# Kernel tuning notes

Hardware: AMD Instinct MI355X
Metric: run time of the kernel (lower is better)

## Reference

```python
import jax, jax.numpy as jnp
import numpy as np

EMB = 1024
HEADS = 16
HEAD_DIM = EMB // HEADS
FF = 4 * EMB


def _gelu_tanh(x):
    c = jnp.sqrt(jnp.asarray(2.0 / jnp.pi, x.dtype))
    return 0.5 * x * (1.0 + jnp.tanh(c * (x + 0.044715 * x ** 3)))


def _layernorm(x, scale, shift, eps=1e-5):
    mean = jnp.mean(x, axis=-1, keepdims=True)
    var = jnp.mean((x - mean) ** 2, axis=-1, keepdims=True)
    return scale * (x - mean) / jnp.sqrt(var + eps) + shift


def setup_inputs() -> dict:
    key = jax.random.key(0)
    ks = jax.random.split(key, 8)
    s = 0.02
    return {
        "x": jax.random.normal(ks[0], (2, 2048, EMB), jnp.float32),
        "w_q": jax.random.normal(ks[1], (EMB, EMB), jnp.float32) * s,
        "w_k": jax.random.normal(ks[2], (EMB, EMB), jnp.float32) * s,
        "w_v": jax.random.normal(ks[3], (EMB, EMB), jnp.float32) * s,
        "w_o": jax.random.normal(ks[4], (EMB, EMB), jnp.float32) * s,
        "b_o": jnp.zeros((EMB,), jnp.float32),
        "ln1_scale": jnp.ones((EMB,), jnp.float32),
        "ln1_shift": jnp.zeros((EMB,), jnp.float32),
        "ln2_scale": jnp.ones((EMB,), jnp.float32),
        "ln2_shift": jnp.zeros((EMB,), jnp.float32),
        "w_ff1": jax.random.normal(ks[5], (EMB, FF), jnp.float32) * s,
        "b_ff1": jnp.zeros((FF,), jnp.float32),
        "w_ff2": jax.random.normal(ks[6], (FF, EMB), jnp.float32) * s,
        "b_ff2": jnp.zeros((EMB,), jnp.float32),
    }


def _attention(x, w_q, w_k, w_v, w_o, b_o):
    b, n, _ = x.shape
    q = (x @ w_q).reshape(b, n, HEADS, HEAD_DIM).transpose(0, 2, 1, 3)  # bhnd
    k = (x @ w_k).reshape(b, n, HEADS, HEAD_DIM).transpose(0, 2, 1, 3)
    v = (x @ w_v).reshape(b, n, HEADS, HEAD_DIM).transpose(0, 2, 1, 3)
    scores = jnp.einsum("bhqd,bhkd->bhqk", q, k)
    causal = jnp.triu(jnp.ones((n, n), bool), k=1)
    scores = jnp.where(causal, -jnp.inf, scores)
    # original scales AFTER masking (-inf stays -inf)
    attn = jax.nn.softmax(scores / jnp.sqrt(jnp.asarray(HEAD_DIM, x.dtype)), axis=-1)
    ctx = jnp.einsum("bhqk,bhkd->bhqd", attn, v)
    ctx = ctx.transpose(0, 2, 1, 3).reshape(b, n, EMB)
    return ctx @ w_o + b_o


def reference(x, w_q, w_k, w_v, w_o, b_o, ln1_scale, ln1_shift,
              ln2_scale, ln2_shift, w_ff1, b_ff1, w_ff2, b_ff2):
    h = _layernorm(x, ln1_scale, ln1_shift)
    h = _attention(h, w_q, w_k, w_v, w_o, b_o)
    x = x + h  # dropout is identity at drop_rate=0 / eval
    h = _layernorm(x, ln2_scale, ln2_shift)
    h = _gelu_tanh(h @ w_ff1 + b_ff1) @ w_ff2 + b_ff2
    return x + h
```

## Files before the change

### kernel.cpp

```cpp
#include <hip/hip_runtime.h>
#include <math.h>

#define EMB 1024
#define HEADS 16
#define HD 64
#define FF_DIM 4096
#define SEQ 2048
#define BATCH 2
#define NTOK (BATCH * SEQ)

typedef __bf16 bf16x8 __attribute__((ext_vector_type(8)));
typedef float f32x4 __attribute__((ext_vector_type(4)));

__device__ __forceinline__ unsigned short f2bf(float f) {
    union { float f; unsigned int u; } v; v.f = f;
    unsigned int r = v.u + 0x7fff + ((v.u >> 16) & 1);
    return (unsigned short)(r >> 16);
}

__device__ __forceinline__ float gelu_f(float x) {
    const float c = 0.7978845608028654f;
    float x3 = x * x * x;
    return 0.5f * x * (1.f + tanhf(c * (x + 0.044715f * x3)));
}

#define GLOAD_LDS16(g, l)                                                      \
    __builtin_amdgcn_global_load_lds(                                          \
        (const __attribute__((address_space(1))) void*)(g),                    \
        (__attribute__((address_space(3))) void*)(l), 16, 0, 0)

__global__ __launch_bounds__(256) void ln_kernel(const float* __restrict__ x,
                                                 const float* __restrict__ scale,
                                                 const float* __restrict__ shift,
                                                 unsigned short* __restrict__ out) {
    int row = blockIdx.x;
    const float* xr = x + (size_t)row * EMB;
    unsigned short* yr = out + (size_t)row * EMB;
    int t = threadIdx.x;

    float v[4];
    float s = 0.f, s2 = 0.f;
#pragma unroll
    for (int i = 0; i < 4; i++) {
        v[i] = xr[t + i * 256];
        s += v[i];
        s2 += v[i] * v[i];
    }
    for (int o = 32; o > 0; o >>= 1) {
        s += __shfl_down(s, o, 64);
        s2 += __shfl_down(s2, o, 64);
    }
    __shared__ float red[4], red2[4];
    int wave = t >> 6;
    if ((t & 63) == 0) { red[wave] = s; red2[wave] = s2; }
    __syncthreads();
    if (t == 0) {
        float a = 0.f, b = 0.f;
#pragma unroll
        for (int i = 0; i < 4; i++) { a += red[i]; b += red2[i]; }
        red[0] = a; red2[0] = b;
    }
    __syncthreads();
    float mean = red[0] * (1.f / EMB);
    float var = red2[0] * (1.f / EMB) - mean * mean;
    float rstd = rsqrtf(var + 1e-5f);
#pragma unroll
    for (int i = 0; i < 4; i++) {
        int c = t + i * 256;
        yr[c] = f2bf(scale[c] * (v[i] - mean) * rstd + shift[c]);
    }
}

__global__ __launch_bounds__(256) void transpose_cast6(
    const float* __restrict__ w0, const float* __restrict__ w1,
    const float* __restrict__ w2, const float* __restrict__ w3,
    const float* __restrict__ w4, const float* __restrict__ w5,
    unsigned short* __restrict__ o0, unsigned short* __restrict__ o1,
    unsigned short* __restrict__ o2, unsigned short* __restrict__ o3,
    unsigned short* __restrict__ o4, unsigned short* __restrict__ o5) {
    __shared__ float tile[64][65];
    int id = blockIdx.x;
    const float* src; unsigned short* dst; int K, N, lid;
    if (id < 256)       { src = w0; dst = o0; K = 1024; N = 1024; lid = id; }
    else if (id < 512)  { src = w1; dst = o1; K = 1024; N = 1024; lid = id - 256; }
    else if (id < 768)  { src = w2; dst = o2; K = 1024; N = 1024; lid = id - 512; }
    else if (id < 1024) { src = w3; dst = o3; K = 1024; N = 1024; lid = id - 768; }
    else if (id < 2048) { src = w4; dst = o4; K = 1024; N = 4096; lid = id - 1024; }
    else                { src = w5; dst = o5; K = 4096; N = 1024; lid = id - 2048; }
    int tn = N >> 6;
    int k0 = (lid / tn) << 6, n0 = (lid % tn) << 6;
    int t = threadIdx.x;
    int rr = t >> 6, cc = t & 63;
#pragma unroll
    for (int i = 0; i < 16; i++) {
        int r = i * 4 + rr;
        tile[r][cc] = src[(size_t)(k0 + r) * N + n0 + cc];
    }
    __syncthreads();
#pragma unroll
    for (int i = 0; i < 16; i++) {
        int r = i * 4 + rr;
        dst[(size_t)(n0 + r) * K + k0 + cc] = f2bf(tile[cc][r]);
    }
}

template <int EPI>
__global__ __launch_bounds__(256) void mfma_gemm(
    const unsigned short* __restrict__ A,
    const unsigned short* __restrict__ Bt,
    void* __restrict__ Cv,
    const float* __restrict__ bias,
    const float* __restrict__ resid,
    int M, int N, int K) {
    __shared__ unsigned short As[128 * 32];
    __shared__ unsigned short Bs[128 * 32];

    const int t = threadIdx.x;
    const int w = t >> 6, lane = t & 63;
    const int m0 = blockIdx.y * 128, n0 = blockIdx.x * 128;

    const int sr0 = (w << 5) + (lane >> 2);
    const int sr1 = sr0 + 16;
    const int p = lane & 3;
    const int c0 = p ^ ((sr0 >> 1) & 3);
    const int c1 = p ^ ((sr1 >> 1) & 3);
    const unsigned short* gA0 = A + (size_t)(m0 + sr0) * K + c0 * 8;
    const unsigned short* gA1 = A + (size_t)(m0 + sr1) * K + c1 * 8;
    const unsigned short* gB0 = Bt + (size_t)(n0 + sr0) * K + c0 * 8;
    const unsigned short* gB1 = Bt + (size_t)(n0 + sr1) * K + c1 * 8;
    unsigned short* lA0 = &As[(w << 5) * 32];
    unsigned short* lA1 = &As[((w << 5) + 16) * 32];
    unsigned short* lB0 = &Bs[(w << 5) * 32];
    unsigned short* lB1 = &Bs[((w << 5) + 16) * 32];

    const int mrow = (w >> 1) * 64, ncol = (w & 1) * 64;
    int aoff[4], boff[4];
#pragma unroll
    for (int i = 0; i < 4; i++) {
        int ra = mrow + i * 16 + (lane & 15);
        int pa = (lane >> 4) ^ ((ra >> 1) & 3);
        aoff[i] = ra * 32 + pa * 8;
        int rb = ncol + i * 16 + (lane & 15);
        int pb = (lane >> 4) ^ ((rb >> 1) & 3);
        boff[i] = rb * 32 + pb * 8;
    }

    f32x4 acc[4][4];
#pragma unroll
    for (int i = 0; i < 4; i++)
#pragma unroll
        for (int j = 0; j < 4; j++) acc[i][j] = (f32x4){0.f, 0.f, 0.f, 0.f};

    for (int k0 = 0; k0 < K; k0 += 32) {
        __syncthreads();
        GLOAD_LDS16(gA0, lA0);
        GLOAD_LDS16(gA1, lA1);
        GLOAD_LDS16(gB0, lB0);
        GLOAD_LDS16(gB1, lB1);
        gA0 += 32; gA1 += 32; gB0 += 32; gB1 += 32;
        __syncthreads();

        bf16x8 af[4], bfr[4];
#pragma unroll
        for (int i = 0; i < 4; i++) {
            af[i] = *reinterpret_cast<const bf16x8*>(&As[aoff[i]]);
            bfr[i] = *reinterpret_cast<const bf16x8*>(&Bs[boff[i]]);
        }
#pragma unroll
        for (int i = 0; i < 4; i++)
#pragma unroll
            for (int j = 0; j < 4; j++)
                acc[i][j] = __builtin_amdgcn_mfma_f32_16x16x32_bf16(
                    af[i], bfr[j], acc[i][j], 0, 0, 0);
    }

    const int ccol = lane & 15;
    const int crow = (lane >> 4) << 2;
#pragma unroll
    for (int i = 0; i < 4; i++) {
#pragma unroll
        for (int j = 0; j < 4; j++) {
            int col = n0 + ncol + j * 16 + ccol;
#pragma unroll
            for (int r = 0; r < 4; r++) {
                int row = m0 + mrow + i * 16 + crow + r;
                size_t idx = (size_t)row * N + col;
                float val = acc[i][j][r];
                if constexpr (EPI == 1) {
                    ((float*)Cv)[idx] = val + bias[col] + resid[idx];
                } else {
                    ((unsigned short*)Cv)[idx] = f2bf(gelu_f(val + bias[col]));
                }
            }
        }
    }
}

__global__ __launch_bounds__(256) void mfma_gemm_pk(
    const unsigned short* __restrict__ A,
    const unsigned short* __restrict__ Bt,
    float* __restrict__ P,
    int M, int N, int K) {
    __shared__ unsigned short As[128 * 32];
    __shared__ unsigned short Bs[128 * 32];

    const int t = threadIdx.x;
    const int w = t >> 6, lane = t & 63;
    const int m0 = blockIdx.y * 128, n0 = blockIdx.x * 128;
    const int kc = K / gridDim.z;
    const int kbeg = blockIdx.z * kc;

    const int sr0 = (w << 5) + (lane >> 2);
    const int sr1 = sr0 + 16;
    const int pp = lane & 3;
    const int c0 = pp ^ ((sr0 >> 1) & 3);
    const int c1 = pp ^ ((sr1 >> 1) & 3);
    const unsigned short* gA0 = A + (size_t)(m0 + sr0) * K + kbeg + c0 * 8;
    const unsigned short* gA1 = A + (size_t)(m0 + sr1) * K + kbeg + c1 * 8;
    const unsigned short* gB0 = Bt + (size_t)(n0 + sr0) * K + kbeg + c0 * 8;
    const unsigned short* gB1 = Bt + (size_t)(n0 + sr1) * K + kbeg + c1 * 8;
    unsigned short* lA0 = &As[(w << 5) * 32];
    unsigned short* lA1 = &As[((w << 5) + 16) * 32];
    unsigned short* lB0 = &Bs[(w << 5) * 32];
    unsigned short* lB1 = &Bs[((w << 5) + 16) * 32];

    const int mrow = (w >> 1) * 64, ncol = (w & 1) * 64;
    int aoff[4], boff[4];
#pragma unroll
    for (int i = 0; i < 4; i++) {
        int ra = mrow + i * 16 + (lane & 15);
        int pa = (lane >> 4) ^ ((ra >> 1) & 3);
        aoff[i] = ra * 32 + pa * 8;
        int rb = ncol + i * 16 + (lane & 15);
        int pb = (lane >> 4) ^ ((rb >> 1) & 3);
        boff[i] = rb * 32 + pb * 8;
    }

    f32x4 acc[4][4];
#pragma unroll
    for (int i = 0; i < 4; i++)
#pragma unroll
        for (int j = 0; j < 4; j++) acc[i][j] = (f32x4){0.f, 0.f, 0.f, 0.f};

    for (int k0 = 0; k0 < kc; k0 += 32) {
        __syncthreads();
        GLOAD_LDS16(gA0, lA0);
        GLOAD_LDS16(gA1, lA1);
        GLOAD_LDS16(gB0, lB0);
        GLOAD_LDS16(gB1, lB1);
        gA0 += 32; gA1 += 32; gB0 += 32; gB1 += 32;
        __syncthreads();

        bf16x8 af[4], bfr[4];
#pragma unroll
        for (int i = 0; i < 4; i++) {
            af[i] = *reinterpret_cast<const bf16x8*>(&As[aoff[i]]);
            bfr[i] = *reinterpret_cast<const bf16x8*>(&Bs[boff[i]]);
        }
#pragma unroll
        for (int i = 0; i < 4; i++)
#pragma unroll
            for (int j = 0; j < 4; j++)
                acc[i][j] = __builtin_amdgcn_mfma_f32_16x16x32_bf16(
                    af[i], bfr[j], acc[i][j], 0, 0, 0);
    }

    float* C = P + (size_t)blockIdx.z * M * N;
    const int ccol = lane & 15;
    const int crow = (lane >> 4) << 2;
#pragma unroll
    for (int i = 0; i < 4; i++) {
#pragma unroll
        for (int j = 0; j < 4; j++) {
            int col = n0 + ncol + j * 16 + ccol;
#pragma unroll
            for (int r = 0; r < 4; r++) {
                int row = m0 + mrow + i * 16 + crow + r;
                C[(size_t)row * N + col] = acc[i][j][r];
            }
        }
    }
}

__global__ __launch_bounds__(256) void oproj_reduce(
    float* __restrict__ out, const float* __restrict__ x,
    const float* __restrict__ p0, const float* __restrict__ p1,
    const float* __restrict__ bias) {
    int i = blockIdx.x * 256 + threadIdx.x;
    float4 xv = ((const float4*)x)[i];
    float4 a = ((const float4*)p0)[i];
    float4 b = ((const float4*)p1)[i];
    int c = (i * 4) & (EMB - 1);
    xv.x += a.x + b.x + bias[c];
    xv.y += a.y + b.y + bias[c + 1];
    xv.z += a.z + b.z + bias[c + 2];
    xv.w += a.w + b.w + bias[c + 3];
    ((float4*)out)[i] = xv;
}

__global__ __launch_bounds__(256) void ff2_reduce(
    float* __restrict__ out, const float* __restrict__ p0,
    const float* __restrict__ p1, const float* __restrict__ bias) {
    int i = blockIdx.x * 256 + threadIdx.x;
    float4 o = ((const float4*)out)[i];
    float4 a = ((const float4*)p0)[i];
    float4 b = ((const float4*)p1)[i];
    int c = (i * 4) & (EMB - 1);
    o.x += a.x + b.x + bias[c];
    o.y += a.y + b.y + bias[c + 1];
    o.z += a.z + b.z + bias[c + 2];
    o.w += a.w + b.w + bias[c + 3];
    ((float4*)out)[i] = o;
}

__global__ __launch_bounds__(256) void qkv_gemm(
    const unsigned short* __restrict__ lnO,
    const unsigned short* __restrict__ wqkT,
    const unsigned short* __restrict__ wvT,
    unsigned short* __restrict__ q,
    unsigned short* __restrict__ kb,
    unsigned short* __restrict__ vT) {
    __shared__ unsigned short As[128 * 32];
    __shared__ unsigned short Bs[128 * 32];

    const int t = threadIdx.x;
    const int w = t >> 6, lane = t & 63;
    const int bid = blockIdx.x;
    const bool qk = bid < 512;

    const unsigned short *A, *Bt;
    int m0, n0, N;
    if (qk) {
        A = lnO; Bt = wqkT;
        m0 = (bid >> 4) * 128; n0 = (bid & 15) * 128; N = 2048;
    } else {
        int lb = bid - 512;
        A = wvT; Bt = lnO;
        m0 = (lb & 7) * 128; n0 = (lb >> 3) * 128; N = 4096;
    }
    const int K = 1024;

    const int sr0 = (w << 5) + (lane >> 2);
    const int sr1 = sr0 + 16;
    const int p = lane & 3;
    const int c0 = p ^ ((sr0 >> 1) & 3);
    const int c1 = p ^ ((sr1 >> 1) & 3);
    const unsigned short* gA0 = A + (size_t)(m0 + sr0) * K + c0 * 8;
    const unsigned short* gA1 = A + (size_t)(m0 + sr1) * K + c1 * 8;
    const unsigned short* gB0 = Bt + (size_t)(n0 + sr0) * K + c0 * 8;
    const unsigned short* gB1 = Bt + (size_t)(n0 + sr1) * K + c1 * 8;
    unsigned short* lA0 = &As[(w << 5) * 32];
    unsigned short* lA1 = &As[((w << 5) + 16) * 32];
    unsigned short* lB0 = &Bs[(w << 5) * 32];
    unsigned short* lB1 = &Bs[((w << 5) + 16) * 32];

    const int mrow = (w >> 1) * 64, ncol = (w & 1) * 64;
    int aoff[4], boff[4];
#pragma unroll
    for (int i = 0; i < 4; i++) {
        int ra = mrow + i * 16 + (lane & 15);
        int pa = (lane >> 4) ^ ((ra >> 1) & 3);
        aoff[i] = ra * 32 + pa * 8;
        int rb = ncol + i * 16 + (lane & 15);
        int pb = (lane >> 4) ^ ((rb >> 1) & 3);
        boff[i] = rb * 32 + pb * 8;
    }

    f32x4 acc[4][4];
#pragma unroll
    for (int i = 0; i < 4; i++)
#pragma unroll
        for (int j = 0; j < 4; j++) acc[i][j] = (f32x4){0.f, 0.f, 0.f, 0.f};

    for (int k0 = 0; k0 < K; k0 += 32) {
        __syncthreads();
        GLOAD_LDS16(gA0, lA0);
        GLOAD_LDS16(gA1, lA1);
        GLOAD_LDS16(gB0, lB0);
        GLOAD_LDS16(gB1, lB1);
        gA0 += 32; gA1 += 32; gB0 += 32; gB1 += 32;
        __syncthreads();

        bf16x8 af[4], bfr[4];
#pragma unroll
        for (int i = 0; i < 4; i++) {
            af[i] = *reinterpret_cast<const bf16x8*>(&As[aoff[i]]);
            bfr[i] = *reinterpret_cast<const bf16x8*>(&Bs[boff[i]]);
        }
#pragma unroll
        for (int i = 0; i < 4; i++)
#pragma unroll
            for (int j = 0; j < 4; j++)
                acc[i][j] = __builtin_amdgcn_mfma_f32_16x16x32_bf16(
                    af[i], bfr[j], acc[i][j], 0, 0, 0);
    }

    const int ccol = lane & 15;
    const int crow = (lane >> 4) << 2;
    unsigned short* dst;
    int nbase;
    if (qk) {
        dst = (n0 < 1024) ? q : kb;
        nbase = n0 & 1023;
    } else {
        dst = vT;
        nbase = n0;
    }
    const int ldc = qk ? 1024 : 4096;
#pragma unroll
    for (int i = 0; i < 4; i++) {
#pragma unroll
        for (int j = 0; j < 4; j++) {
            int col = nbase + ncol + j * 16 + ccol;
#pragma unroll
            for (int r = 0; r < 4; r++) {
                int row = m0 + mrow + i * 16 + crow + r;
                dst[(size_t)row * ldc + col] = f2bf(acc[i][j][r]);
            }
        }
    }
}

__global__ __launch_bounds__(256) void attn_mfma(
    const unsigned short* __restrict__ Q,
    const unsigned short* __restrict__ K,
    const unsigned short* __restrict__ Vt,
    unsigned short* __restrict__ O) {
    __shared__ unsigned short Ks[2][64 * 64];
    __shared__ unsigned short Vs[2][64 * 64];
    __shared__ unsigned short Ps[4][16 * 64];

    const int t = threadIdx.x;
    const int w = t >> 6, lane = t & 63;
    const int l15 = lane & 15, l4 = lane >> 4;
    const int bh = blockIdx.y;
    const int b = bh >> 4, h = bh & 15;
    const int pair = blockIdx.x;

    const int sr = (w << 3) + (lane >> 3);
    const int sc = lane & 7;
    const int c = sc ^ (sr & 7);
    const unsigned short* kbase = K + ((size_t)(b * SEQ)) * EMB + h * HD;
    const unsigned short* vbase = Vt + ((size_t)(h * HD)) * (size_t)NTOK + (size_t)b * SEQ;
    unsigned short* Pw = &Ps[w][0];

#define STAGE(k0s, buf)                                                        \
    do {                                                                       \
        GLOAD_LDS16(kbase + (size_t)((k0s) + sr) * EMB + c * 8,                \
                    &Ks[buf][(w << 3) * 64]);                                  \
        GLOAD_LDS16(kbase + (size_t)((k0s) + sr + 32) * EMB + c * 8,           \
                    &Ks[buf][((w << 3) + 32) * 64]);                           \
        GLOAD_LDS16(vbase + (size_t)sr * NTOK + (k0s) + c * 8,                 \
                    &Vs[buf][(w << 3) * 64]);                                  \
        GLOAD_LDS16(vbase + (size_t)(sr + 32) * NTOK + (k0s) + c * 8,          \
                    &Vs[buf][((w << 3) + 32) * 64]);                           \
    } while (0)

    const float C1 = 0.125f * 1.4426950408889634f;
    const float C2 = 3.0f * 1.4426950408889634f;

#pragma unroll
    for (int phase = 0; phase < 2; phase++) {
        const int qt = phase ? pair : (31 - pair);
        const int q0 = qt * 64;

        const unsigned short* qg =
            Q + ((size_t)(b * SEQ + q0 + w * 16 + l15)) * EMB + h * HD + l4 * 8;
        bf16x8 qf0 = *(const bf16x8*)qg;
        bf16x8 qf1 = *(const bf16x8*)(qg + 32);
        const int qrow_c = q0 + w * 16 + l4 * 4;

        float lsum[4] = {0.f, 0.f, 0.f, 0.f};
        f32x4 Oacc[4];
#pragma unroll
        for (int j = 0; j < 4; j++) Oacc[j] = (f32x4){0.f, 0.f, 0.f, 0.f};

        const int ntiles = qt + 1;
        __syncthreads();
        STAGE(0, 0);
        for (int tile = 0; tile < ntiles; tile++) {
            const int k0 = tile * 64;
            const int buf = tile & 1;
            __syncthreads();
            if (tile + 1 < ntiles) STAGE(k0 + 64, buf ^ 1);

            f32x4 S[4];
#pragma unroll
            for (int j = 0; j < 4; j++) S[j] = (f32x4){0.f, 0.f, 0.f, 0.f};
#pragma unroll
            for (int s = 0; s < 2; s++) {
                bf16x8 qf = s ? qf1 : qf0;
#pragma unroll
                for (int j = 0; j < 4; j++) {
                    int rk = 16 * j + l15;
                    int phys = (s * 4 + l4) ^ (rk & 7);
                    bf16x8 kf = *(const bf16x8*)&Ks[buf][rk * 64 + phys * 8];
                    S[j] = __builtin_amdgcn_mfma_f32_16x16x32_bf16(qf, kf, S[j], 0, 0, 0);
                }
            }

            if (tile == ntiles - 1) {
#pragma unroll
                for (int j = 0; j < 4; j++)
#pragma unroll
                    for (int r = 0; r < 4; r++) {
                        float e = exp2f(S[j][r] * C1 - C2);
                        if (k0 + 16 * j + l15 > qrow_c + r) e = 0.f;
                        S[j][r] = e;
                        lsum[r] += e;
                    }
            } else {
#pragma unroll
                for (int j = 0; j < 4; j++)
#pragma unroll
                    for (int r = 0; r < 4; r++) {
                        float e = exp2f(S[j][r] * C1 - C2);
                        S[j][r] = e;
                        lsum[r] += e;
                    }
            }

#pragma unroll
            for (int r = 0; r < 4; r++) {
                int row = l4 * 4 + r;
#pragma unroll
                for (int j = 0; j < 4; j++) {
                    int col = 16 * j + l15;
                    int phys = (col >> 3) ^ (row & 7);
                    Pw[row * 64 + phys * 8 + (col & 7)] = f2bf(S[j][r]);
                }
            }

#pragma unroll
            for (int s = 0; s < 2; s++) {
                int pphys = (s * 4 + l4) ^ (l15 & 7);
                bf16x8 pf = *(const bf16x8*)&Pw[l15 * 64 + pphys * 8];
#pragma unroll
                for (int j = 0; j < 4; j++) {
                    int rv = 16 * j + l15;
                    int vphys = (s * 4 + l4) ^ (rv & 7);
                    bf16x8 vf = *(const bf16x8*)&Vs[buf][rv * 64 + vphys * 8];
                    Oacc[j] = __builtin_amdgcn_mfma_f32_16x16x32_bf16(pf, vf, Oacc[j], 0, 0, 0);
                }
            }
        }

#pragma unroll
        for (int r = 0; r < 4; r++) {
            float l = lsum[r];
#pragma unroll
            for (int off = 1; off < 16; off <<= 1)
                l += __shfl_xor(l, off, 64);
            float inv = 1.f / l;
            size_t rowb = (size_t)(b * SEQ + qrow_c + r) * EMB + h * HD;
#pragma unroll
            for (int j = 0; j < 4; j++)
                O[rowb + 16 * j + l15] = f2bf(Oacc[j][r] * inv);
        }
    }
#undef STAGE
}

extern "C" void kernel_launch(void* const* d_in, const int* in_sizes, int n_in,
                              void* d_out, int out_size, void* d_ws, size_t ws_size,
                              hipStream_t stream) {
    const float* x     = (const float*)d_in[0];
    const float* w_q   = (const float*)d_in[1];
    const float* w_k   = (const float*)d_in[2];
    const float* w_v   = (const float*)d_in[3];
    const float* w_o   = (const float*)d_in[4];
    const float* b_o   = (const float*)d_in[5];
    const float* ln1s  = (const float*)d_in[6];
    const float* ln1b  = (const float*)d_in[7];
    const float* ln2s  = (const float*)d_in[8];
    const float* ln2b  = (const float*)d_in[9];
    const float* w_ff1 = (const float*)d_in[10];
    const float* b_ff1 = (const float*)d_in[11];
    const float* w_ff2 = (const float*)d_in[12];
    const float* b_ff2 = (const float*)d_in[13];
    float* out = (float*)d_out;

    char* p = (char*)d_ws;
    unsigned short* lnO  = (unsigned short*)p; p += (size_t)NTOK * EMB * 2;
    unsigned short* q    = (unsigned short*)p; p += (size_t)NTOK * EMB * 2;
    unsigned short* kbuf = (unsigned short*)p; p += (size_t)NTOK * EMB * 2;
    unsigned short* vT   = (unsigned short*)p; p += (size_t)NTOK * EMB * 2;
    unsigned short* ctx  = (unsigned short*)p; p += (size_t)NTOK * EMB * 2;
    unsigned short* ff1a = (unsigned short*)p; p += (size_t)NTOK * FF_DIM * 2;
    unsigned short* wqkT = (unsigned short*)p; p += (size_t)2 * EMB * EMB * 2;
    unsigned short* wvT  = (unsigned short*)p; p += (size_t)EMB * EMB * 2;
    unsigned short* woT  = (unsigned short*)p; p += (size_t)EMB * EMB * 2;
    unsigned short* wf1T = (unsigned short*)p; p += (size_t)FF_DIM * EMB * 2;
    unsigned short* wf2T = (unsigned short*)p; p += (size_t)EMB * FF_DIM * 2;

    float* pbuf = (float*)lnO;

    dim3 blk(256);
    dim3 gOproj(EMB / 128, NTOK / 128, 2);
    dim3 gFF1(FF_DIM / 128, NTOK / 128);
    dim3 gFF2(EMB / 128, NTOK / 128, 2);
    dim3 gAttn(16, BATCH * HEADS);

    transpose_cast6<<<3072, blk, 0, stream>>>(
        w_q, w_k, w_v, w_o, w_ff1, w_ff2,
        wqkT, wqkT + (size_t)EMB * EMB, wvT, woT, wf1T, wf2T);
    ln_kernel<<<NTOK, blk, 0, stream>>>(x, ln1s, ln1b, lnO);
    qkv_gemm<<<768, blk, 0, stream>>>(lnO, wqkT, wvT, q, kbuf, vT);
    attn_mfma<<<gAttn, blk, 0, stream>>>(q, kbuf, vT, ctx);
    mfma_gemm_pk<<<gOproj, blk, 0, stream>>>(ctx, woT, pbuf, NTOK, EMB, EMB);
    oproj_reduce<<<NTOK * EMB / 4 / 256, blk, 0, stream>>>(
        out, x, pbuf, pbuf + (size_t)NTOK * EMB, b_o);
    ln_kernel<<<NTOK, blk, 0, stream>>>(out, ln2s, ln2b, lnO);
    mfma_gemm<2><<<gFF1, blk, 0, stream>>>(lnO, wf1T, ff1a, b_ff1, nullptr, NTOK, FF_DIM, EMB);
    mfma_gemm_pk<<<gFF2, blk, 0, stream>>>(ff1a, wf2T, pbuf, NTOK, EMB, FF_DIM);
    ff2_reduce<<<NTOK * EMB / 4 / 256, blk, 0, stream>>>(
        out, pbuf, pbuf + (size_t)NTOK * EMB, b_ff2);
}
```

Before: 397.9 us.

## Fuse o-proj reduction with LN2, use sigmoid GELU, split-K 4 for FF2

Replaces the o-proj partial reduction and the second layernorm with one kernel that sums partials, bias and residual, writes the residual, and emits the bf16 LN output. GELU is rewritten via the sigmoid identity with a fast exp and reciprocal. FF2 split-K is raised to 4 when the workspace has room for extra partial buffers, with a four-way reduce. This trades extra partial-sum traffic for more parallelism and saves a full activation round trip plus a launch.

```diff
diff --git a/kernel.cpp b/kernel.cpp
--- a/kernel.cpp
+++ b/kernel.cpp
@@ -19,9 +19,10 @@
 }
 
 __device__ __forceinline__ float gelu_f(float x) {
-    const float c = 0.7978845608028654f;
-    float x3 = x * x * x;
-    return 0.5f * x * (1.f + tanhf(c * (x + 0.044715f * x3)));
+    const float A = 1.5957691216057308f;
+    const float B = 0.07135481282989427f;
+    float zz = x * (A + B * x * x);
+    return x * __builtin_amdgcn_rcpf(1.f + __expf(-zz));
 }
 
 #define GLOAD_LDS16(g, l)                                                      \
@@ -68,6 +69,51 @@
     for (int i = 0; i < 4; i++) {
         int c = t + i * 256;
         yr[c] = f2bf(scale[c] * (v[i] - mean) * rstd + shift[c]);
+    }
+}
+
+__global__ __launch_bounds__(256) void oproj_ln(
+    const float* __restrict__ x, const float* __restrict__ p0,
+    const float* __restrict__ p1, const float* __restrict__ bo,
+    const float* __restrict__ scale, const float* __restrict__ shift,
+    float* __restrict__ out, unsigned short* __restrict__ ln2O) {
+    int row = blockIdx.x;
+    size_t rb = (size_t)row * EMB;
+    int t = threadIdx.x;
+
+    float v[4];
+    float s = 0.f, s2 = 0.f;
+#pragma unroll
+    for (int i = 0; i < 4; i++) {
+        int c = t + i * 256;
+        float val = x[rb + c] + p0[rb + c] + p1[rb + c] + bo[c];
+        out[rb + c] = val;
+        v[i] = val;
+        s += val;
+        s2 += val * val;
+    }
+    for (int o = 32; o > 0; o >>= 1) {
+        s += __shfl_down(s, o, 64);
+        s2 += __shfl_down(s2, o, 64);
+    }
+    __shared__ float red[4], red2[4];
+    int wave = t >> 6;
+    if ((t & 63) == 0) { red[wave] = s; red2[wave] = s2; }
+    __syncthreads();
+    if (t == 0) {
+        float a = 0.f, b = 0.f;
+#pragma unroll
+        for (int i = 0; i < 4; i++) { a += red[i]; b += red2[i]; }
+        red[0] = a; red2[0] = b;
+    }
+    __syncthreads();
+    float mean = red[0] * (1.f / EMB);
+    float var = red2[0] * (1.f / EMB) - mean * mean;
+    float rstd = rsqrtf(var + 1e-5f);
+#pragma unroll
+    for (int i = 0; i < 4; i++) {
+        int c = t + i * 256;
+        ln2O[rb + c] = f2bf(scale[c] * (v[i] - mean) * rstd + shift[c]);
     }
 }
 
@@ -199,7 +245,7 @@
 __global__ __launch_bounds__(256) void mfma_gemm_pk(
     const unsigned short* __restrict__ A,
     const unsigned short* __restrict__ Bt,
-    float* __restrict__ P,
+    float* __restrict__ P0, float* __restrict__ P1,
     int M, int N, int K) {
     __shared__ unsigned short As[128 * 32];
     __shared__ unsigned short Bs[128 * 32];
@@ -265,7 +311,8 @@
                     af[i], bfr[j], acc[i][j], 0, 0, 0);
     }
 
-    float* C = P + (size_t)blockIdx.z * M * N;
+    float* C = (blockIdx.z < 2) ? (P0 + (size_t)blockIdx.z * M * N)
+                                : (P1 + (size_t)(blockIdx.z - 2) * M * N);
     const int ccol = lane & 15;
     const int crow = (lane >> 4) << 2;
 #pragma unroll
@@ -282,23 +329,7 @@
     }
 }
 
-__global__ __launch_bounds__(256) void oproj_reduce(
-    float* __restrict__ out, const float* __restrict__ x,
-    const float* __restrict__ p0, const float* __restrict__ p1,
-    const float* __restrict__ bias) {
-    int i = blockIdx.x * 256 + threadIdx.x;
-    float4 xv = ((const float4*)x)[i];
-    float4 a = ((const float4*)p0)[i];
-    float4 b = ((const float4*)p1)[i];
-    int c = (i * 4) & (EMB - 1);
-    xv.x += a.x + b.x + bias[c];
-    xv.y += a.y + b.y + bias[c + 1];
-    xv.z += a.z + b.z + bias[c + 2];
-    xv.w += a.w + b.w + bias[c + 3];
-    ((float4*)out)[i] = xv;
-}
-
-__global__ __launch_bounds__(256) void ff2_reduce(
+__global__ __launch_bounds__(256) void ff2_reduce2(
     float* __restrict__ out, const float* __restrict__ p0,
     const float* __restrict__ p1, const float* __restrict__ bias) {
     int i = blockIdx.x * 256 + threadIdx.x;
@@ -310,6 +341,24 @@
     o.y += a.y + b.y + bias[c + 1];
     o.z += a.z + b.z + bias[c + 2];
     o.w += a.w + b.w + bias[c + 3];
+    ((float4*)out)[i] = o;
+}
+
+__global__ __launch_bounds__(256) void ff2_reduce4(
+    float* __restrict__ out, const float* __restrict__ p0,
+    const float* __restrict__ p1, const float* __restrict__ p2,
+    const float* __restrict__ p3, const float* __restrict__ bias) {
+    int i = blockIdx.x * 256 + threadIdx.x;
+    float4 o = ((const float4*)out)[i];
+    float4 a = ((const float4*)p0)[i];
+    float4 b = ((const float4*)p1)[i];
+    float4 d = ((const float4*)p2)[i];
+    float4 e = ((const float4*)p3)[i];
+    int c = (i * 4) & (EMB - 1);
+    o.x += a.x + b.x + d.x + e.x + bias[c];
+    o.y += a.y + b.y + d.y + e.y + bias[c + 1];
+    o.z += a.z + b.z + d.z + e.z + bias[c + 2];
+    o.w += a.w + b.w + d.w + e.w + bias[c + 3];
     ((float4*)out)[i] = o;
 }
 
@@ -594,11 +643,15 @@
     unsigned short* wf2T = (unsigned short*)p; p += (size_t)EMB * FF_DIM * 2;
 
     float* pbuf = (float*)lnO;
+    size_t used = (size_t)(p - (char*)d_ws);
+    size_t pkbytes = 2 * (size_t)NTOK * EMB * sizeof(float);
+    bool z4 = ws_size >= used + pkbytes;
+    float* pex = (float*)p;
 
     dim3 blk(256);
     dim3 gOproj(EMB / 128, NTOK / 128, 2);
     dim3 gFF1(FF_DIM / 128, NTOK / 128);
-    dim3 gFF2(EMB / 128, NTOK / 128, 2);
+    dim3 gFF2(EMB / 128, NTOK / 128, z4 ? 4 : 2);
     dim3 gAttn(16, BATCH * HEADS);
 
     transpose_cast6<<<3072, blk, 0, stream>>>(
@@ -607,12 +660,16 @@
     ln_kernel<<<NTOK, blk, 0, stream>>>(x, ln1s, ln1b, lnO);
     qkv_gemm<<<768, blk, 0, stream>>>(lnO, wqkT, wvT, q, kbuf, vT);
     attn_mfma<<<gAttn, blk, 0, stream>>>(q, kbuf, vT, ctx);
-    mfma_gemm_pk<<<gOproj, blk, 0, stream>>>(ctx, woT, pbuf, NTOK, EMB, EMB);
-    oproj_reduce<<<NTOK * EMB / 4 / 256, blk, 0, stream>>>(
-        out, x, pbuf, pbuf + (size_t)NTOK * EMB, b_o);
-    ln_kernel<<<NTOK, blk, 0, stream>>>(out, ln2s, ln2b, lnO);
-    mfma_gemm<2><<<gFF1, blk, 0, stream>>>(lnO, wf1T, ff1a, b_ff1, nullptr, NTOK, FF_DIM, EMB);
-    mfma_gemm_pk<<<gFF2, blk, 0, stream>>>(ff1a, wf2T, pbuf, NTOK, EMB, FF_DIM);
-    ff2_reduce<<<NTOK * EMB / 4 / 256, blk, 0, stream>>>(
-        out, pbuf, pbuf + (size_t)NTOK * EMB, b_ff2);
-}
+    mfma_gemm_pk<<<gOproj, blk, 0, stream>>>(ctx, woT, pbuf, nullptr, NTOK, EMB, EMB);
+    oproj_ln<<<NTOK, blk, 0, stream>>>(
+        x, pbuf, pbuf + (size_t)NTOK * EMB, b_o, ln2s, ln2b, out, ctx);
+    mfma_gemm<2><<<gFF1, blk, 0, stream>>>(ctx, wf1T, ff1a, b_ff1, nullptr, NTOK, FF_DIM, EMB);
+    mfma_gemm_pk<<<gFF2, blk, 0, stream>>>(ff1a, wf2T, pbuf, pex, NTOK, EMB, FF_DIM);
+    if (z4) {
+        ff2_reduce4<<<NTOK * EMB / 4 / 256, blk, 0, stream>>>(
+            out, pbuf, pbuf + (size_t)NTOK * EMB, pex, pex + (size_t)NTOK * EMB, b_ff2);
+    } else {
+        ff2_reduce2<<<NTOK * EMB / 4 / 256, blk, 0, stream>>>(
+            out, pbuf, pbuf + (size_t)NTOK * EMB, b_ff2);
+    }
+}
```

Measured after the change: 383.2 us. -3.7%, faster.
